# Kernel tuning notes

Hardware: AMD Instinct MI355X
Metric: run time of the kernel (lower is better)

The kernel has to match this reference:

```python
import jax, jax.numpy as jnp
import numpy as np

H = 2048      # hidden_size
E = 16        # num_experts
I = 512       # moe_intermediate_size
IS = 2048     # shared_expert_intermediate_size
TOP_K = 2
B, S = 1, 2048


def setup_inputs() -> dict:
    key = jax.random.key(0)
    ks = jax.random.split(key, 9)
    std = 0.02
    return {
        "hidden_states": jax.random.normal(ks[0], (B, S, H), dtype=jnp.float32),
        "gate_w": jax.random.normal(ks[1], (E, H), dtype=jnp.float32) * std,
        "w1": jax.random.normal(ks[2], (E, I, H), dtype=jnp.float32) * std,  # gate_proj per expert
        "w2": jax.random.normal(ks[3], (E, H, I), dtype=jnp.float32) * std,  # down_proj per expert
        "w3": jax.random.normal(ks[4], (E, I, H), dtype=jnp.float32) * std,  # up_proj per expert
        "ws_gate": jax.random.normal(ks[5], (IS, H), dtype=jnp.float32) * std,  # shared gate_proj
        "ws_up": jax.random.normal(ks[6], (IS, H), dtype=jnp.float32) * std,    # shared up_proj
        "ws_down": jax.random.normal(ks[7], (H, IS), dtype=jnp.float32) * std,  # shared down_proj
        "shared_gate_w": jax.random.normal(ks[8], (1, H), dtype=jnp.float32) * std,
    }


def reference(hidden_states, gate_w, w1, w2, w3, ws_gate, ws_up, ws_down, shared_gate_w):
    b, s, h = hidden_states.shape
    x = hidden_states.reshape(-1, h)                     # [T, H]
    T = x.shape[0]

    # Router: softmax in fp32, top-k, renormalize (norm_topk_prob=True)
    router_logits = x @ gate_w.T                         # [T, E]
    routing = jax.nn.softmax(router_logits.astype(jnp.float32), axis=-1)
    topw, sel = jax.lax.top_k(routing, TOP_K)            # [T, K]
    topw = topw / jnp.sum(topw, axis=-1, keepdims=True)
    topw = topw.astype(x.dtype)

    # Scatter top-k weights into dense [T, E] combine matrix (torch_moe semantics)
    combine = jnp.zeros((T, E), dtype=x.dtype).at[jnp.arange(T)[:, None], sel].set(topw)

    # Expert SwiGLU MLPs evaluated densely, masked/weighted by combine
    hmid = jax.nn.silu(jnp.einsum('th,eih->tei', x, w1)) * jnp.einsum('th,eih->tei', x, w3)  # [T,E,I]
    hmid = hmid * combine[:, :, None]
    moe_out = jnp.einsum('tei,ehi->th', hmid, w2)        # [T, H]

    # Shared expert with sigmoid gate
    shared = (jax.nn.silu(x @ ws_gate.T) * (x @ ws_up.T)) @ ws_down.T  # [T, H]
    shared = jax.nn.sigmoid(x @ shared_gate_w.T) * shared

    return (moe_out + shared).reshape(b, s, h)
```

## Files before the change

### kernel.cpp

```cpp
#include <hip/hip_runtime.h>
#include <hip/hip_bf16.h>
#include <cmath>

#define HDIM 2048
#define NEXP 16
#define IDIM 512
#define ISDIM 2048
#define NTOK 2048
#define MAXTILES 80
#define ROWSCAP (MAXTILES * 64)

typedef short bf16x8 __attribute__((ext_vector_type(8)));
typedef float f32x4 __attribute__((ext_vector_type(4)));

__device__ __forceinline__ unsigned short f2bf(float f) {
  unsigned int u = __builtin_bit_cast(unsigned int, f);
  u += 0x7FFFu + ((u >> 16) & 1u);
  return (unsigned short)(u >> 16);
}

__device__ __forceinline__ void stage_w8(const float* __restrict__ src,
                                         unsigned short* __restrict__ dst) {
  const float4* p = reinterpret_cast<const float4*>(src);
  float4 a = p[0];
  float4 b = p[1];
  bf16x8 v = {(short)f2bf(a.x), (short)f2bf(a.y), (short)f2bf(a.z), (short)f2bf(a.w),
              (short)f2bf(b.x), (short)f2bf(b.y), (short)f2bf(b.z), (short)f2bf(b.w)};
  *reinterpret_cast<bf16x8*>(dst) = v;
}

__global__ __launch_bounds__(256) void k_prep(const float* __restrict__ x,
                                              unsigned short* __restrict__ xb,
                                              int* __restrict__ counts) {
  int i = blockIdx.x * 256 + threadIdx.x;
  float4 v = reinterpret_cast<const float4*>(x)[i];
  ushort4 o;
  o.x = f2bf(v.x); o.y = f2bf(v.y); o.z = f2bf(v.z); o.w = f2bf(v.w);
  reinterpret_cast<ushort4*>(xb)[i] = o;
  if (blockIdx.x == 0 && threadIdx.x < NEXP) counts[threadIdx.x] = 0;
}

__global__ __launch_bounds__(256) void k_router(const float* __restrict__ x,
                                                const float* __restrict__ gate_w,
                                                const float* __restrict__ sgw,
                                                int* __restrict__ sel,
                                                float* __restrict__ wnorm,
                                                float* __restrict__ sig,
                                                int* __restrict__ counts) {
  __shared__ float xs[HDIM];
  __shared__ float logits[NEXP];
  __shared__ float red[4];
  int t = blockIdx.x;
  int tid = threadIdx.x;
  for (int i = tid; i < HDIM / 4; i += 256) {
    float4 v = reinterpret_cast<const float4*>(x + (size_t)t * HDIM)[i];
    xs[i * 4 + 0] = v.x; xs[i * 4 + 1] = v.y; xs[i * 4 + 2] = v.z; xs[i * 4 + 3] = v.w;
  }
  __syncthreads();
  int e = tid >> 4, j = tid & 15;
  float p = 0.f;
  const float* gw = gate_w + (size_t)e * HDIM;
  for (int i = j; i < HDIM; i += 16) p += xs[i] * gw[i];
  for (int off = 8; off; off >>= 1) p += __shfl_xor(p, off, 16);
  if (j == 0) logits[e] = p;
  float q = 0.f;
  for (int i = tid; i < HDIM; i += 256) q += xs[i] * sgw[i];
  for (int off = 32; off; off >>= 1) q += __shfl_xor(q, off, 64);
  int wid = tid >> 6;
  if ((tid & 63) == 0) red[wid] = q;
  __syncthreads();
  if (tid == 0) {
    float sq = red[0] + red[1] + red[2] + red[3];
    sig[t] = 1.f / (1.f + expf(-sq));
    float m = logits[0];
    for (int i = 1; i < NEXP; i++) m = fmaxf(m, logits[i]);
    float pe[NEXP];
    for (int i = 0; i < NEXP; i++) pe[i] = expf(logits[i] - m);
    int i1 = 0; float v1 = pe[0];
    for (int i = 1; i < NEXP; i++) if (pe[i] > v1) { v1 = pe[i]; i1 = i; }
    int i2 = (i1 == 0) ? 1 : 0; float v2 = pe[i2];
    for (int i = 0; i < NEXP; i++)
      if (i != i1 && i != i2 && pe[i] > v2) { v2 = pe[i]; i2 = i; }
    float tw = v1 + v2;
    sel[t * 2] = i1; sel[t * 2 + 1] = i2;
    wnorm[t * 2] = v1 / tw; wnorm[t * 2 + 1] = v2 / tw;
    atomicAdd(&counts[i1], 1);
    atomicAdd(&counts[i2], 1);
  }
}

__global__ __launch_bounds__(256) void k_scan(const int* __restrict__ counts,
                                              int* __restrict__ offs,
                                              int* __restrict__ tile_expert,
                                              int* __restrict__ row_token,
                                              int* __restrict__ fillpos) {
  int tid = threadIdx.x;
  if (tid == 0) {
    int acc = 0;
    for (int e = 0; e < NEXP; e++) {
      offs[e] = acc;
      int nt = (counts[e] + 63) >> 6;
      for (int i = 0; i < nt; i++) tile_expert[(acc >> 6) + i] = e;
      acc += nt << 6;
    }
    for (int m = acc >> 6; m < MAXTILES; m++) tile_expert[m] = -1;
  }
  for (int r = tid; r < ROWSCAP; r += 256) row_token[r] = -1;
  if (tid < NEXP) fillpos[tid] = 0;
}

__global__ __launch_bounds__(256) void k_scatter(const int* __restrict__ sel,
                                                 const int* __restrict__ offs,
                                                 int* __restrict__ fillpos,
                                                 int* __restrict__ row_token,
                                                 int* __restrict__ tok2row) {
  int t = blockIdx.x * 256 + threadIdx.x;
  for (int k = 0; k < 2; k++) {
    int e = sel[t * 2 + k];
    int pos = atomicAdd(&fillpos[e], 1);
    int row = offs[e] + pos;
    row_token[row] = t;
    tok2row[t * 2 + k] = row;
  }
}

__global__ __launch_bounds__(256) void k_expert_gu(
    const unsigned short* __restrict__ xb, const float* __restrict__ w1,
    const float* __restrict__ w3, const int* __restrict__ tile_expert,
    const int* __restrict__ row_token, unsigned short* __restrict__ hmid) {
  int mt = blockIdx.y, nt = blockIdx.x;
  int e = tile_expert[mt];
  if (e < 0) return;
  __shared__ unsigned short As[64 * 72];
  __shared__ unsigned short Bg[64 * 72];
  __shared__ unsigned short Bu[64 * 72];
  __shared__ int toks[64];
  int tid = threadIdx.x;
  if (tid < 64) {
    int tk = row_token[mt * 64 + tid];
    toks[tid] = tk < 0 ? 0 : tk;
  }
  const float* w1e = w1 + ((size_t)e * IDIM + nt * 64) * HDIM;
  const float* w3e = w3 + ((size_t)e * IDIM + nt * 64) * HDIM;
  int wave = tid >> 6, lane = tid & 63;
  int wm = wave >> 1, wn = wave & 1;
  int quad = lane >> 4, l16 = lane & 15;
  int r0 = tid >> 3, kof0 = (tid & 7) << 3;
  int c2 = tid + 256;
  int r1 = c2 >> 3, kof1 = (c2 & 7) << 3;
  f32x4 accG[2][2] = {};
  f32x4 accU[2][2] = {};
  __syncthreads();
  for (int k0 = 0; k0 < HDIM; k0 += 64) {
    *reinterpret_cast<bf16x8*>(&As[r0 * 72 + kof0]) =
        *reinterpret_cast<const bf16x8*>(xb + (size_t)toks[r0] * HDIM + k0 + kof0);
    *reinterpret_cast<bf16x8*>(&As[r1 * 72 + kof1]) =
        *reinterpret_cast<const bf16x8*>(xb + (size_t)toks[r1] * HDIM + k0 + kof1);
    stage_w8(w1e + (size_t)r0 * HDIM + k0 + kof0, &Bg[r0 * 72 + kof0]);
    stage_w8(w1e + (size_t)r1 * HDIM + k0 + kof1, &Bg[r1 * 72 + kof1]);
    stage_w8(w3e + (size_t)r0 * HDIM + k0 + kof0, &Bu[r0 * 72 + kof0]);
    stage_w8(w3e + (size_t)r1 * HDIM + k0 + kof1, &Bu[r1 * 72 + kof1]);
    __syncthreads();
#pragma unroll
    for (int ks = 0; ks < 2; ks++) {
      bf16x8 af[2], bg[2], bu[2];
#pragma unroll
      for (int ms = 0; ms < 2; ms++)
        af[ms] = *reinterpret_cast<const bf16x8*>(
            &As[(wm * 32 + ms * 16 + l16) * 72 + ks * 32 + quad * 8]);
#pragma unroll
      for (int ns = 0; ns < 2; ns++) {
        bg[ns] = *reinterpret_cast<const bf16x8*>(
            &Bg[(wn * 32 + ns * 16 + l16) * 72 + ks * 32 + quad * 8]);
        bu[ns] = *reinterpret_cast<const bf16x8*>(
            &Bu[(wn * 32 + ns * 16 + l16) * 72 + ks * 32 + quad * 8]);
      }
#pragma unroll
      for (int ms = 0; ms < 2; ms++)
#pragma unroll
        for (int ns = 0; ns < 2; ns++) {
          accG[ms][ns] = __builtin_amdgcn_mfma_f32_16x16x32_bf16(af[ms], bg[ns], accG[ms][ns], 0, 0, 0);
          accU[ms][ns] = __builtin_amdgcn_mfma_f32_16x16x32_bf16(af[ms], bu[ns], accU[ms][ns], 0, 0, 0);
        }
    }
    __syncthreads();
  }
#pragma unroll
  for (int ms = 0; ms < 2; ms++)
#pragma unroll
    for (int ns = 0; ns < 2; ns++)
#pragma unroll
      for (int r = 0; r < 4; r++) {
        float g = accG[ms][ns][r], u = accU[ms][ns][r];
        float hv = (g / (1.f + __expf(-g))) * u;
        int row = mt * 64 + wm * 32 + ms * 16 + quad * 4 + r;
        int col = nt * 64 + wn * 32 + ns * 16 + l16;
        hmid[(size_t)row * IDIM + col] = f2bf(hv);
      }
}

__global__ __launch_bounds__(256) void k_expert_down(
    const unsigned short* __restrict__ hmid, const float* __restrict__ w2,
    const int* __restrict__ tile_expert, float* __restrict__ moe_rows) {
  int mt = blockIdx.y, nt = blockIdx.x;
  int e = tile_expert[mt];
  if (e < 0) return;
  __shared__ unsigned short As[64 * 72];
  __shared__ unsigned short Bs[64 * 72];
  int tid = threadIdx.x;
  const float* w2e = w2 + ((size_t)e * HDIM + nt * 64) * IDIM;
  int wave = tid >> 6, lane = tid & 63;
  int wm = wave >> 1, wn = wave & 1;
  int quad = lane >> 4, l16 = lane & 15;
  int r0 = tid >> 3, kof0 = (tid & 7) << 3;
  int c2 = tid + 256;
  int r1 = c2 >> 3, kof1 = (c2 & 7) << 3;
  f32x4 acc[2][2] = {};
  for (int k0 = 0; k0 < IDIM; k0 += 64) {
    *reinterpret_cast<bf16x8*>(&As[r0 * 72 + kof0]) =
        *reinterpret_cast<const bf16x8*>(hmid + (size_t)(mt * 64 + r0) * IDIM + k0 + kof0);
    *reinterpret_cast<bf16x8*>(&As[r1 * 72 + kof1]) =
        *reinterpret_cast<const bf16x8*>(hmid + (size_t)(mt * 64 + r1) * IDIM + k0 + kof1);
    stage_w8(w2e + (size_t)r0 * IDIM + k0 + kof0, &Bs[r0 * 72 + kof0]);
    stage_w8(w2e + (size_t)r1 * IDIM + k0 + kof1, &Bs[r1 * 72 + kof1]);
    __syncthreads();
#pragma unroll
    for (int ks = 0; ks < 2; ks++) {
      bf16x8 af[2], bf[2];
#pragma unroll
      for (int ms = 0; ms < 2; ms++)
        af[ms] = *reinterpret_cast<const bf16x8*>(
            &As[(wm * 32 + ms * 16 + l16) * 72 + ks * 32 + quad * 8]);
#pragma unroll
      for (int ns = 0; ns < 2; ns++)
        bf[ns] = *reinterpret_cast<const bf16x8*>(
            &Bs[(wn * 32 + ns * 16 + l16) * 72 + ks * 32 + quad * 8]);
#pragma unroll
      for (int ms = 0; ms < 2; ms++)
#pragma unroll
        for (int ns = 0; ns < 2; ns++)
          acc[ms][ns] = __builtin_amdgcn_mfma_f32_16x16x32_bf16(af[ms], bf[ns], acc[ms][ns], 0, 0, 0);
    }
    __syncthreads();
  }
#pragma unroll
  for (int ms = 0; ms < 2; ms++)
#pragma unroll
    for (int ns = 0; ns < 2; ns++)
#pragma unroll
      for (int r = 0; r < 4; r++) {
        int row = mt * 64 + wm * 32 + ms * 16 + quad * 4 + r;
        int col = nt * 64 + wn * 32 + ns * 16 + l16;
        moe_rows[(size_t)row * HDIM + col] = acc[ms][ns][r];
      }
}

__global__ __launch_bounds__(256) void k_shared_gu(
    const unsigned short* __restrict__ xb, const float* __restrict__ wg,
    const float* __restrict__ wu, unsigned short* __restrict__ hs) {
  int mt = blockIdx.y, nt = blockIdx.x;
  __shared__ unsigned short As[64 * 72];
  __shared__ unsigned short Bg[64 * 72];
  __shared__ unsigned short Bu[64 * 72];
  int tid = threadIdx.x;
  const float* wge = wg + (size_t)(nt * 64) * HDIM;
  const float* wue = wu + (size_t)(nt * 64) * HDIM;
  int wave = tid >> 6, lane = tid & 63;
  int wm = wave >> 1, wn = wave & 1;
  int quad = lane >> 4, l16 = lane & 15;
  int r0 = tid >> 3, kof0 = (tid & 7) << 3;
  int c2 = tid + 256;
  int r1 = c2 >> 3, kof1 = (c2 & 7) << 3;
  f32x4 accG[2][2] = {};
  f32x4 accU[2][2] = {};
  for (int k0 = 0; k0 < HDIM; k0 += 64) {
    *reinterpret_cast<bf16x8*>(&As[r0 * 72 + kof0]) =
        *reinterpret_cast<const bf16x8*>(xb + (size_t)(mt * 64 + r0) * HDIM + k0 + kof0);
    *reinterpret_cast<bf16x8*>(&As[r1 * 72 + kof1]) =
        *reinterpret_cast<const bf16x8*>(xb + (size_t)(mt * 64 + r1) * HDIM + k0 + kof1);
    stage_w8(wge + (size_t)r0 * HDIM + k0 + kof0, &Bg[r0 * 72 + kof0]);
    stage_w8(wge + (size_t)r1 * HDIM + k0 + kof1, &Bg[r1 * 72 + kof1]);
    stage_w8(wue + (size_t)r0 * HDIM + k0 + kof0, &Bu[r0 * 72 + kof0]);
    stage_w8(wue + (size_t)r1 * HDIM + k0 + kof1, &Bu[r1 * 72 + kof1]);
    __syncthreads();
#pragma unroll
    for (int ks = 0; ks < 2; ks++) {
      bf16x8 af[2], bg[2], bu[2];
#pragma unroll
      for (int ms = 0; ms < 2; ms++)
        af[ms] = *reinterpret_cast<const bf16x8*>(
            &As[(wm * 32 + ms * 16 + l16) * 72 + ks * 32 + quad * 8]);
#pragma unroll
      for (int ns = 0; ns < 2; ns++) {
        bg[ns] = *reinterpret_cast<const bf16x8*>(
            &Bg[(wn * 32 + ns * 16 + l16) * 72 + ks * 32 + quad * 8]);
        bu[ns] = *reinterpret_cast<const bf16x8*>(
            &Bu[(wn * 32 + ns * 16 + l16) * 72 + ks * 32 + quad * 8]);
      }
#pragma unroll
      for (int ms = 0; ms < 2; ms++)
#pragma unroll
        for (int ns = 0; ns < 2; ns++) {
          accG[ms][ns] = __builtin_amdgcn_mfma_f32_16x16x32_bf16(af[ms], bg[ns], accG[ms][ns], 0, 0, 0);
          accU[ms][ns] = __builtin_amdgcn_mfma_f32_16x16x32_bf16(af[ms], bu[ns], accU[ms][ns], 0, 0, 0);
        }
    }
    __syncthreads();
  }
#pragma unroll
  for (int ms = 0; ms < 2; ms++)
#pragma unroll
    for (int ns = 0; ns < 2; ns++)
#pragma unroll
      for (int r = 0; r < 4; r++) {
        float g = accG[ms][ns][r], u = accU[ms][ns][r];
        float hv = (g / (1.f + __expf(-g))) * u;
        int row = mt * 64 + wm * 32 + ms * 16 + quad * 4 + r;
        int col = nt * 64 + wn * 32 + ns * 16 + l16;
        hs[(size_t)row * ISDIM + col] = f2bf(hv);
      }
}

__global__ __launch_bounds__(256) void k_shared_down(
    const unsigned short* __restrict__ hs, const float* __restrict__ wsd,
    const float* __restrict__ moe_rows, const int* __restrict__ tok2row,
    const float* __restrict__ wnorm, const float* __restrict__ sig,
    float* __restrict__ out) {
  int mt = blockIdx.y, nt = blockIdx.x;
  __shared__ unsigned short As[64 * 72];
  __shared__ unsigned short Bs[64 * 72];
  int tid = threadIdx.x;
  const float* wsde = wsd + (size_t)(nt * 64) * ISDIM;
  int wave = tid >> 6, lane = tid & 63;
  int wm = wave >> 1, wn = wave & 1;
  int quad = lane >> 4, l16 = lane & 15;
  int r0 = tid >> 3, kof0 = (tid & 7) << 3;
  int c2 = tid + 256;
  int r1 = c2 >> 3, kof1 = (c2 & 7) << 3;
  f32x4 acc[2][2] = {};
  for (int k0 = 0; k0 < ISDIM; k0 += 64) {
    *reinterpret_cast<bf16x8*>(&As[r0 * 72 + kof0]) =
        *reinterpret_cast<const bf16x8*>(hs + (size_t)(mt * 64 + r0) * ISDIM + k0 + kof0);
    *reinterpret_cast<bf16x8*>(&As[r1 * 72 + kof1]) =
        *reinterpret_cast<const bf16x8*>(hs + (size_t)(mt * 64 + r1) * ISDIM + k0 + kof1);
    stage_w8(wsde + (size_t)r0 * ISDIM + k0 + kof0, &Bs[r0 * 72 + kof0]);
    stage_w8(wsde + (size_t)r1 * ISDIM + k0 + kof1, &Bs[r1 * 72 + kof1]);
    __syncthreads();
#pragma unroll
    for (int ks = 0; ks < 2; ks++) {
      bf16x8 af[2], bf[2];
#pragma unroll
      for (int ms = 0; ms < 2; ms++)
        af[ms] = *reinterpret_cast<const bf16x8*>(
            &As[(wm * 32 + ms * 16 + l16) * 72 + ks * 32 + quad * 8]);
#pragma unroll
      for (int ns = 0; ns < 2; ns++)
        bf[ns] = *reinterpret_cast<const bf16x8*>(
            &Bs[(wn * 32 + ns * 16 + l16) * 72 + ks * 32 + quad * 8]);
#pragma unroll
      for (int ms = 0; ms < 2; ms++)
#pragma unroll
        for (int ns = 0; ns < 2; ns++)
          acc[ms][ns] = __builtin_amdgcn_mfma_f32_16x16x32_bf16(af[ms], bf[ns], acc[ms][ns], 0, 0, 0);
    }
    __syncthreads();
  }
#pragma unroll
  for (int ms = 0; ms < 2; ms++)
#pragma unroll
    for (int ns = 0; ns < 2; ns++)
#pragma unroll
      for (int r = 0; r < 4; r++) {
        int t = mt * 64 + wm * 32 + ms * 16 + quad * 4 + r;
        int col = nt * 64 + wn * 32 + ns * 16 + l16;
        float v = acc[ms][ns][r] * sig[t];
        int ra = tok2row[t * 2], rb = tok2row[t * 2 + 1];
        v += wnorm[t * 2] * moe_rows[(size_t)ra * HDIM + col] +
             wnorm[t * 2 + 1] * moe_rows[(size_t)rb * HDIM + col];
        out[(size_t)t * HDIM + col] = v;
      }
}

extern "C" void kernel_launch(void* const* d_in, const int* in_sizes, int n_in,
                              void* d_out, int out_size, void* d_ws, size_t ws_size,
                              hipStream_t stream) {
  const float* x = (const float*)d_in[0];
  const float* gate_w = (const float*)d_in[1];
  const float* w1 = (const float*)d_in[2];
  const float* w2 = (const float*)d_in[3];
  const float* w3 = (const float*)d_in[4];
  const float* wsg = (const float*)d_in[5];
  const float* wsu = (const float*)d_in[6];
  const float* wsd = (const float*)d_in[7];
  const float* sgw = (const float*)d_in[8];
  float* out = (float*)d_out;

  unsigned short* xb = (unsigned short*)d_ws;
  unsigned short* hs = xb + (size_t)NTOK * HDIM;
  unsigned short* hmid = hs + (size_t)NTOK * ISDIM;
  float* moe_rows = (float*)(hmid + (size_t)ROWSCAP * IDIM);
  float* wnorm = moe_rows + (size_t)ROWSCAP * HDIM;
  float* sig = wnorm + 2 * NTOK;
  int* sel = (int*)(sig + NTOK);
  int* tok2row = sel + 2 * NTOK;
  int* row_token = tok2row + 2 * NTOK;
  int* counts = row_token + ROWSCAP;
  int* offs = counts + NEXP;
  int* fillpos = offs + NEXP;
  int* tile_expert = fillpos + NEXP;

  k_prep<<<dim3((NTOK * HDIM) / 1024), dim3(256), 0, stream>>>(x, xb, counts);
  k_router<<<dim3(NTOK), dim3(256), 0, stream>>>(x, gate_w, sgw, sel, wnorm, sig, counts);
  k_scan<<<dim3(1), dim3(256), 0, stream>>>(counts, offs, tile_expert, row_token, fillpos);
  k_scatter<<<dim3(NTOK / 256), dim3(256), 0, stream>>>(sel, offs, fillpos, row_token, tok2row);
  k_expert_gu<<<dim3(IDIM / 64, MAXTILES), dim3(256), 0, stream>>>(
      xb, w1, w3, tile_expert, row_token, hmid);
  k_expert_down<<<dim3(HDIM / 64, MAXTILES), dim3(256), 0, stream>>>(
      hmid, w2, tile_expert, moe_rows);
  k_shared_gu<<<dim3(ISDIM / 64, NTOK / 64), dim3(256), 0, stream>>>(xb, wsg, wsu, hs);
  k_shared_down<<<dim3(HDIM / 64, NTOK / 64), dim3(256), 0, stream>>>(
      hs, wsd, moe_rows, tok2row, wnorm, sig, out);
}
```

Measured before the change: 511.4 us.

## Fuse router with bf16 cast, merge scan/scatter, combine expert and shared gate-up GEMMs

Folds the fp32-to-bf16 cast of x into the router, which now handles four tokens per block with one wave each and gets the top-2 weights directly from a logit-difference sigmoid. Merges the scan and scatter kernels into one block that keeps offsets and fill counters in shared memory. Launches the expert and shared gate/up GEMMs as a single grid so both run concurrently and fill the GPU better. Together these cut launch count and idle tails between small kernels, at the cost of a serial single-block scatter and divergent block roles inside one kernel.

After: 482.4 us. -5.7%, faster.

```diff
diff --git a/kernel.cpp b/kernel.cpp
--- a/kernel.cpp
+++ b/kernel.cpp
@@ -9,6 +9,8 @@
 #define NTOK 2048
 #define MAXTILES 80
 #define ROWSCAP (MAXTILES * 64)
+#define NB_EXP 640
+#define NB_SH 1024
 
 typedef short bf16x8 __attribute__((ext_vector_type(8)));
 typedef float f32x4 __attribute__((ext_vector_type(4)));
@@ -29,119 +31,125 @@
   *reinterpret_cast<bf16x8*>(dst) = v;
 }
 
-__global__ __launch_bounds__(256) void k_prep(const float* __restrict__ x,
-                                              unsigned short* __restrict__ xb,
-                                              int* __restrict__ counts) {
-  int i = blockIdx.x * 256 + threadIdx.x;
-  float4 v = reinterpret_cast<const float4*>(x)[i];
-  ushort4 o;
-  o.x = f2bf(v.x); o.y = f2bf(v.y); o.z = f2bf(v.z); o.w = f2bf(v.w);
-  reinterpret_cast<ushort4*>(xb)[i] = o;
-  if (blockIdx.x == 0 && threadIdx.x < NEXP) counts[threadIdx.x] = 0;
-}
-
 __global__ __launch_bounds__(256) void k_router(const float* __restrict__ x,
                                                 const float* __restrict__ gate_w,
                                                 const float* __restrict__ sgw,
+                                                unsigned short* __restrict__ xb,
                                                 int* __restrict__ sel,
                                                 float* __restrict__ wnorm,
                                                 float* __restrict__ sig,
                                                 int* __restrict__ counts) {
-  __shared__ float xs[HDIM];
-  __shared__ float logits[NEXP];
-  __shared__ float red[4];
-  int t = blockIdx.x;
-  int tid = threadIdx.x;
-  for (int i = tid; i < HDIM / 4; i += 256) {
-    float4 v = reinterpret_cast<const float4*>(x + (size_t)t * HDIM)[i];
-    xs[i * 4 + 0] = v.x; xs[i * 4 + 1] = v.y; xs[i * 4 + 2] = v.z; xs[i * 4 + 3] = v.w;
-  }
-  __syncthreads();
-  int e = tid >> 4, j = tid & 15;
-  float p = 0.f;
-  const float* gw = gate_w + (size_t)e * HDIM;
-  for (int i = j; i < HDIM; i += 16) p += xs[i] * gw[i];
-  for (int off = 8; off; off >>= 1) p += __shfl_xor(p, off, 16);
-  if (j == 0) logits[e] = p;
-  float q = 0.f;
-  for (int i = tid; i < HDIM; i += 256) q += xs[i] * sgw[i];
-  for (int off = 32; off; off >>= 1) q += __shfl_xor(q, off, 64);
-  int wid = tid >> 6;
-  if ((tid & 63) == 0) red[wid] = q;
-  __syncthreads();
-  if (tid == 0) {
-    float sq = red[0] + red[1] + red[2] + red[3];
-    sig[t] = 1.f / (1.f + expf(-sq));
-    float m = logits[0];
-    for (int i = 1; i < NEXP; i++) m = fmaxf(m, logits[i]);
-    float pe[NEXP];
-    for (int i = 0; i < NEXP; i++) pe[i] = expf(logits[i] - m);
-    int i1 = 0; float v1 = pe[0];
-    for (int i = 1; i < NEXP; i++) if (pe[i] > v1) { v1 = pe[i]; i1 = i; }
-    int i2 = (i1 == 0) ? 1 : 0; float v2 = pe[i2];
+  __shared__ float lg[4][17];
+  int tid = threadIdx.x, wid = tid >> 6, lane = tid & 63;
+  int t = blockIdx.x * 4 + wid;
+  const float4* xrow = reinterpret_cast<const float4*>(x + (size_t)t * HDIM);
+  float4 xv[8];
+#pragma unroll
+  for (int s = 0; s < 8; s++) xv[s] = xrow[s * 64 + lane];
+  ushort4* xbrow = reinterpret_cast<ushort4*>(xb + (size_t)t * HDIM);
+#pragma unroll
+  for (int s = 0; s < 8; s++) {
+    ushort4 o;
+    o.x = f2bf(xv[s].x); o.y = f2bf(xv[s].y); o.z = f2bf(xv[s].z); o.w = f2bf(xv[s].w);
+    xbrow[s * 64 + lane] = o;
+  }
+#pragma unroll 1
+  for (int e = 0; e < 17; e++) {
+    const float4* gr =
+        reinterpret_cast<const float4*>(e < 16 ? gate_w + (size_t)e * HDIM : sgw);
+    float acc = 0.f;
+#pragma unroll
+    for (int s = 0; s < 8; s++) {
+      float4 g = gr[s * 64 + lane];
+      acc += xv[s].x * g.x + xv[s].y * g.y + xv[s].z * g.z + xv[s].w * g.w;
+    }
+#pragma unroll
+    for (int off = 32; off; off >>= 1) acc += __shfl_xor(acc, off, 64);
+    if (lane == 0) lg[wid][e] = acc;
+  }
+  if (lane == 0) {
+    float* L = lg[wid];
+    int i1 = 0; float v1 = L[0];
+    for (int i = 1; i < NEXP; i++) if (L[i] > v1) { v1 = L[i]; i1 = i; }
+    int i2 = (i1 == 0) ? 1 : 0; float v2 = L[i2];
     for (int i = 0; i < NEXP; i++)
-      if (i != i1 && i != i2 && pe[i] > v2) { v2 = pe[i]; i2 = i; }
-    float tw = v1 + v2;
-    sel[t * 2] = i1; sel[t * 2 + 1] = i2;
-    wnorm[t * 2] = v1 / tw; wnorm[t * 2 + 1] = v2 / tw;
+      if (i != i1 && i != i2 && L[i] > v2) { v2 = L[i]; i2 = i; }
+    float wa = 1.f / (1.f + expf(v2 - v1));
+    sel[2 * t] = i1; sel[2 * t + 1] = i2;
+    wnorm[2 * t] = wa; wnorm[2 * t + 1] = 1.f - wa;
+    sig[t] = 1.f / (1.f + expf(-L[16]));
     atomicAdd(&counts[i1], 1);
     atomicAdd(&counts[i2], 1);
   }
 }
 
-__global__ __launch_bounds__(256) void k_scan(const int* __restrict__ counts,
-                                              int* __restrict__ offs,
-                                              int* __restrict__ tile_expert,
-                                              int* __restrict__ row_token,
-                                              int* __restrict__ fillpos) {
+__global__ __launch_bounds__(256) void k_scan_scatter(const int* __restrict__ counts,
+                                                      const int* __restrict__ sel,
+                                                      int* __restrict__ tile_expert,
+                                                      int* __restrict__ row_token,
+                                                      int* __restrict__ tok2row) {
+  __shared__ int offs_s[NEXP];
+  __shared__ int fill_s[NEXP];
   int tid = threadIdx.x;
+  for (int r = tid; r < ROWSCAP; r += 256) row_token[r] = -1;
+  if (tid < NEXP) fill_s[tid] = 0;
   if (tid == 0) {
     int acc = 0;
     for (int e = 0; e < NEXP; e++) {
-      offs[e] = acc;
+      offs_s[e] = acc;
       int nt = (counts[e] + 63) >> 6;
       for (int i = 0; i < nt; i++) tile_expert[(acc >> 6) + i] = e;
       acc += nt << 6;
     }
     for (int m = acc >> 6; m < MAXTILES; m++) tile_expert[m] = -1;
   }
-  for (int r = tid; r < ROWSCAP; r += 256) row_token[r] = -1;
-  if (tid < NEXP) fillpos[tid] = 0;
-}
-
-__global__ __launch_bounds__(256) void k_scatter(const int* __restrict__ sel,
-                                                 const int* __restrict__ offs,
-                                                 int* __restrict__ fillpos,
-                                                 int* __restrict__ row_token,
-                                                 int* __restrict__ tok2row) {
-  int t = blockIdx.x * 256 + threadIdx.x;
-  for (int k = 0; k < 2; k++) {
-    int e = sel[t * 2 + k];
-    int pos = atomicAdd(&fillpos[e], 1);
-    int row = offs[e] + pos;
-    row_token[row] = t;
-    tok2row[t * 2 + k] = row;
-  }
-}
-
-__global__ __launch_bounds__(256) void k_expert_gu(
+  __syncthreads();
+  for (int t = tid; t < NTOK; t += 256) {
+    for (int k = 0; k < 2; k++) {
+      int e = sel[2 * t + k];
+      int pos = atomicAdd(&fill_s[e], 1);
+      int row = offs_s[e] + pos;
+      row_token[row] = t;
+      tok2row[2 * t + k] = row;
+    }
+  }
+}
+
+__global__ __launch_bounds__(256) void k_gu(
     const unsigned short* __restrict__ xb, const float* __restrict__ w1,
-    const float* __restrict__ w3, const int* __restrict__ tile_expert,
-    const int* __restrict__ row_token, unsigned short* __restrict__ hmid) {
-  int mt = blockIdx.y, nt = blockIdx.x;
-  int e = tile_expert[mt];
-  if (e < 0) return;
+    const float* __restrict__ w3, const float* __restrict__ wsg,
+    const float* __restrict__ wsu, const int* __restrict__ tile_expert,
+    const int* __restrict__ row_token, unsigned short* __restrict__ hmid,
+    unsigned short* __restrict__ hs) {
   __shared__ unsigned short As[64 * 72];
   __shared__ unsigned short Bg[64 * 72];
   __shared__ unsigned short Bu[64 * 72];
   __shared__ int toks[64];
-  int tid = threadIdx.x;
-  if (tid < 64) {
-    int tk = row_token[mt * 64 + tid];
-    toks[tid] = tk < 0 ? 0 : tk;
-  }
-  const float* w1e = w1 + ((size_t)e * IDIM + nt * 64) * HDIM;
-  const float* w3e = w3 + ((size_t)e * IDIM + nt * 64) * HDIM;
+  int bid = blockIdx.x, tid = threadIdx.x;
+  const float *bGp, *bUp;
+  unsigned short* outp;
+  int ostride, mt, ncol;
+  if (bid < NB_EXP) {
+    mt = bid >> 3;
+    int nt = bid & 7;
+    int e = tile_expert[mt];
+    if (e < 0) return;
+    if (tid < 64) {
+      int tk = row_token[mt * 64 + tid];
+      toks[tid] = tk < 0 ? 0 : tk;
+    }
+    bGp = w1 + ((size_t)e * IDIM + nt * 64) * HDIM;
+    bUp = w3 + ((size_t)e * IDIM + nt * 64) * HDIM;
+    outp = hmid; ostride = IDIM; ncol = nt * 64;
+  } else {
+    int sb = bid - NB_EXP;
+    mt = sb >> 5;
+    int nt = sb & 31;
+    if (tid < 64) toks[tid] = mt * 64 + tid;
+    bGp = wsg + (size_t)(nt * 64) * HDIM;
+    bUp = wsu + (size_t)(nt * 64) * HDIM;
+    outp = hs; ostride = ISDIM; ncol = nt * 64;
+  }
   int wave = tid >> 6, lane = tid & 63;
   int wm = wave >> 1, wn = wave & 1;
   int quad = lane >> 4, l16 = lane & 15;
@@ -156,10 +164,10 @@
         *reinterpret_cast<const bf16x8*>(xb + (size_t)toks[r0] * HDIM + k0 + kof0);
     *reinterpret_cast<bf16x8*>(&As[r1 * 72 + kof1]) =
         *reinterpret_cast<const bf16x8*>(xb + (size_t)toks[r1] * HDIM + k0 + kof1);
-    stage_w8(w1e + (size_t)r0 * HDIM + k0 + kof0, &Bg[r0 * 72 + kof0]);
-    stage_w8(w1e + (size_t)r1 * HDIM + k0 + kof1, &Bg[r1 * 72 + kof1]);
-    stage_w8(w3e + (size_t)r0 * HDIM + k0 + kof0, &Bu[r0 * 72 + kof0]);
-    stage_w8(w3e + (size_t)r1 * HDIM + k0 + kof1, &Bu[r1 * 72 + kof1]);
+    stage_w8(bGp + (size_t)r0 * HDIM + k0 + kof0, &Bg[r0 * 72 + kof0]);
+    stage_w8(bGp + (size_t)r1 * HDIM + k0 + kof1, &Bg[r1 * 72 + kof1]);
+    stage_w8(bUp + (size_t)r0 * HDIM + k0 + kof0, &Bu[r0 * 72 + kof0]);
+    stage_w8(bUp + (size_t)r1 * HDIM + k0 + kof1, &Bu[r1 * 72 + kof1]);
     __syncthreads();
 #pragma unroll
     for (int ks = 0; ks < 2; ks++) {
@@ -194,8 +202,8 @@
         float g = accG[ms][ns][r], u = accU[ms][ns][r];
         float hv = (g / (1.f + __expf(-g))) * u;
         int row = mt * 64 + wm * 32 + ms * 16 + quad * 4 + r;
-        int col = nt * 64 + wn * 32 + ns * 16 + l16;
-        hmid[(size_t)row * IDIM + col] = f2bf(hv);
+        int col = ncol + wn * 32 + ns * 16 + l16;
+        outp[(size_t)row * ostride + col] = f2bf(hv);
       }
 }
 
@@ -255,72 +263,6 @@
       }
 }
 
-__global__ __launch_bounds__(256) void k_shared_gu(
-    const unsigned short* __restrict__ xb, const float* __restrict__ wg,
-    const float* __restrict__ wu, unsigned short* __restrict__ hs) {
-  int mt = blockIdx.y, nt = blockIdx.x;
-  __shared__ unsigned short As[64 * 72];
-  __shared__ unsigned short Bg[64 * 72];
-  __shared__ unsigned short Bu[64 * 72];
-  int tid = threadIdx.x;
-  const float* wge = wg + (size_t)(nt * 64) * HDIM;
-  const float* wue = wu + (size_t)(nt * 64) * HDIM;
-  int wave = tid >> 6, lane = tid & 63;
-  int wm = wave >> 1, wn = wave & 1;
-  int quad = lane >> 4, l16 = lane & 15;
-  int r0 = tid >> 3, kof0 = (tid & 7) << 3;
-  int c2 = tid + 256;
-  int r1 = c2 >> 3, kof1 = (c2 & 7) << 3;
-  f32x4 accG[2][2] = {};
-  f32x4 accU[2][2] = {};
-  for (int k0 = 0; k0 < HDIM; k0 += 64) {
-    *reinterpret_cast<bf16x8*>(&As[r0 * 72 + kof0]) =
-        *reinterpret_cast<const bf16x8*>(xb + (size_t)(mt * 64 + r0) * HDIM + k0 + kof0);
-    *reinterpret_cast<bf16x8*>(&As[r1 * 72 + kof1]) =
-        *reinterpret_cast<const bf16x8*>(xb + (size_t)(mt * 64 + r1) * HDIM + k0 + kof1);
-    stage_w8(wge + (size_t)r0 * HDIM + k0 + kof0, &Bg[r0 * 72 + kof0]);
-    stage_w8(wge + (size_t)r1 * HDIM + k0 + kof1, &Bg[r1 * 72 + kof1]);
-    stage_w8(wue + (size_t)r0 * HDIM + k0 + kof0, &Bu[r0 * 72 + kof0]);
-    stage_w8(wue + (size_t)r1 * HDIM + k0 + kof1, &Bu[r1 * 72 + kof1]);
-    __syncthreads();
-#pragma unroll
-    for (int ks = 0; ks < 2; ks++) {
-      bf16x8 af[2], bg[2], bu[2];
-#pragma unroll
-      for (int ms = 0; ms < 2; ms++)
-        af[ms] = *reinterpret_cast<const bf16x8*>(
-            &As[(wm * 32 + ms * 16 + l16) * 72 + ks * 32 + quad * 8]);
-#pragma unroll
-      for (int ns = 0; ns < 2; ns++) {
-        bg[ns] = *reinterpret_cast<const bf16x8*>(
-            &Bg[(wn * 32 + ns * 16 + l16) * 72 + ks * 32 + quad * 8]);
-        bu[ns] = *reinterpret_cast<const bf16x8*>(
-            &Bu[(wn * 32 + ns * 16 + l16) * 72 + ks * 32 + quad * 8]);
-      }
-#pragma unroll
-      for (int ms = 0; ms < 2; ms++)
-#pragma unroll
-        for (int ns = 0; ns < 2; ns++) {
-          accG[ms][ns] = __builtin_amdgcn_mfma_f32_16x16x32_bf16(af[ms], bg[ns], accG[ms][ns], 0, 0, 0);
-          accU[ms][ns] = __builtin_amdgcn_mfma_f32_16x16x32_bf16(af[ms], bu[ns], accU[ms][ns], 0, 0, 0);
-        }
-    }
-    __syncthreads();
-  }
-#pragma unroll
-  for (int ms = 0; ms < 2; ms++)
-#pragma unroll
-    for (int ns = 0; ns < 2; ns++)
-#pragma unroll
-      for (int r = 0; r < 4; r++) {
-        float g = accG[ms][ns][r], u = accU[ms][ns][r];
-        float hv = (g / (1.f + __expf(-g))) * u;
-        int row = mt * 64 + wm * 32 + ms * 16 + quad * 4 + r;
-        int col = nt * 64 + wn * 32 + ns * 16 + l16;
-        hs[(size_t)row * ISDIM + col] = f2bf(hv);
-      }
-}
-
 __global__ __launch_bounds__(256) void k_shared_down(
     const unsigned short* __restrict__ hs, const float* __restrict__ wsd,
     const float* __restrict__ moe_rows, const int* __restrict__ tok2row,
@@ -405,19 +347,17 @@
   int* tok2row = sel + 2 * NTOK;
   int* row_token = tok2row + 2 * NTOK;
   int* counts = row_token + ROWSCAP;
-  int* offs = counts + NEXP;
-  int* fillpos = offs + NEXP;
-  int* tile_expert = fillpos + NEXP;
-
-  k_prep<<<dim3((NTOK * HDIM) / 1024), dim3(256), 0, stream>>>(x, xb, counts);
-  k_router<<<dim3(NTOK), dim3(256), 0, stream>>>(x, gate_w, sgw, sel, wnorm, sig, counts);
-  k_scan<<<dim3(1), dim3(256), 0, stream>>>(counts, offs, tile_expert, row_token, fillpos);
-  k_scatter<<<dim3(NTOK / 256), dim3(256), 0, stream>>>(sel, offs, fillpos, row_token, tok2row);
-  k_expert_gu<<<dim3(IDIM / 64, MAXTILES), dim3(256), 0, stream>>>(
-      xb, w1, w3, tile_expert, row_token, hmid);
+  int* tile_expert = counts + NEXP;
+
+  hipMemsetAsync(counts, 0, NEXP * sizeof(int), stream);
+  k_router<<<dim3(NTOK / 4), dim3(256), 0, stream>>>(x, gate_w, sgw, xb, sel, wnorm,
+                                                     sig, counts);
+  k_scan_scatter<<<dim3(1), dim3(256), 0, stream>>>(counts, sel, tile_expert,
+                                                    row_token, tok2row);
+  k_gu<<<dim3(NB_EXP + NB_SH), dim3(256), 0, stream>>>(xb, w1, w3, wsg, wsu,
+                                                       tile_expert, row_token, hmid, hs);
   k_expert_down<<<dim3(HDIM / 64, MAXTILES), dim3(256), 0, stream>>>(
       hmid, w2, tile_expert, moe_rows);
-  k_shared_gu<<<dim3(ISDIM / 64, NTOK / 64), dim3(256), 0, stream>>>(xb, wsg, wsu, hs);
   k_shared_down<<<dim3(HDIM / 64, NTOK / 64), dim3(256), 0, stream>>>(
       hs, wsd, moe_rows, tok2row, wnorm, sig, out);
 }
```
